# Kernel optimization log

Measured on AMD Instinct MI355X. Metric: run time of the kernel, lower is better.

The kernel has to match this reference:

```python
import jax, jax.numpy as jnp
import numpy as np

DIM = 144
HEADS = 6
HEAD_DIM = DIM // HEADS
SCALE = HEAD_DIM ** -0.5
WS = (2, 8, 8)  # (T, H, W); N = 2*8*8 = 128


def _rel_pos_index(ws):
    d, h, w = ws
    coords = np.stack(np.meshgrid(np.arange(d), np.arange(h), np.arange(w), indexing='ij'))
    cf = coords.reshape(3, -1)                      # (3, N)
    rc = (cf[:, :, None] - cf[:, None, :]).transpose(1, 2, 0)  # (N, N, 3)
    rc[..., 0] += d - 1
    rc[..., 1] += h - 1
    rc[..., 2] += w - 1
    rc[..., 0] *= (2 * h - 1) * (2 * w - 1)
    rc[..., 1] *= (2 * w - 1)
    return rc.sum(-1)                               # (N, N) int


def _sine_pos_encoding(hw, num_pos_feats, temperature=10000.0):
    # matches get_sine_position_encoding(..., normalize=True) -> (1, H*W, 2*num_pos_feats)
    H, W = hw
    scale = 2.0 * np.pi
    ones = np.ones((1, H, W), dtype=np.float64)
    y = np.cumsum(ones, 1)
    x = np.cumsum(ones, 2)
    eps = 1e-6
    y = y / (y[:, -1:, :] + eps) * scale
    x = x / (x[:, :, -1:] + eps) * scale
    dim_t = np.arange(num_pos_feats, dtype=np.float64)
    dim_t = temperature ** (2.0 * (dim_t // 2) / num_pos_feats)
    pos_x = x[..., None] / dim_t
    pos_y = y[..., None] / dim_t
    pos_x = np.stack((np.sin(pos_x[..., 0::2]), np.cos(pos_x[..., 1::2])), -1).reshape(1, H, W, -1)
    pos_y = np.stack((np.sin(pos_y[..., 0::2]), np.cos(pos_y[..., 1::2])), -1).reshape(1, H, W, -1)
    pos = np.concatenate((pos_y, pos_x), 3)         # (1, H, W, 2*npf)
    return pos.reshape(1, H * W, 2 * num_pos_feats).astype(np.float32)


RPI = _rel_pos_index(WS)                              # (128, 128) numpy int const
POS = _sine_pos_encoding(WS[1:], DIM // 2)            # (1, 64, 144) numpy const


def setup_inputs() -> dict:
    key = jax.random.key(0)
    ks = jax.random.split(key, 6)
    wB, N, C = 1024, 128, DIM
    return {
        'x': jax.random.normal(ks[0], (wB, N, C), jnp.float32),
        'rpb_table': 0.02 * jax.random.normal(ks[1], (675, HEADS), jnp.float32),
        'w_qkv_self': jax.random.normal(ks[2], (3 * C, C), jnp.float32) * (C ** -0.5),
        'w_qkv_mut': jax.random.normal(ks[3], (3 * C, C), jnp.float32) * (C ** -0.5),
        'w_proj': jax.random.normal(ks[4], (C, 2 * C), jnp.float32) * ((2 * C) ** -0.5),
        'b_proj': jax.random.normal(ks[5], (C,), jnp.float32) * 0.01,
    }


def _qkv(x, w):
    wB, N, C = x.shape
    qkv = (x @ w.T).reshape(wB, N, 3, HEADS, HEAD_DIM).transpose(2, 0, 3, 1, 4)
    return qkv[0], qkv[1], qkv[2]  # each (wB, heads, N, head_dim)


def _attention(q, k, v, rpb=None):
    # q,k,v: (wB, heads, n, head_dim)
    beta = jnp.einsum('bhnd,bhmd->bhnm', q * SCALE, k)
    if rpb is not None:
        beta = beta + rpb                             # (1, heads, n, n) broadcast
    alpha = jax.nn.softmax(beta, axis=-1)
    out = jnp.einsum('bhnm,bhmd->bhnd', alpha, v)
    wB, _, n, _ = q.shape
    return out.transpose(0, 2, 1, 3).reshape(wB, n, HEADS * HEAD_DIM)


def reference(x, rpb_table, w_qkv_self, w_qkv_mut, w_proj, b_proj):
    wB, N, C = x.shape
    # --- self attention with relative position bias ---
    q, k, v = _qkv(x, w_qkv_self)
    rpb = rpb_table[jnp.asarray(RPI.reshape(-1))].reshape(N, N, HEADS)
    rpb = rpb.transpose(2, 0, 1)[None]                # (1, heads, N, N)
    x_out = _attention(q, k, v, rpb)                  # (wB, N, C)
    # --- mutual attention between the two temporal halves ---
    pos = jnp.tile(jnp.asarray(POS, x.dtype), (1, 2, 1))  # (1, N, C)
    qm, km, vm = _qkv(x + pos, w_qkv_mut)
    half = N // 2
    q1, q2 = qm[:, :, :half], qm[:, :, half:]
    k1, k2 = km[:, :, :half], km[:, :, half:]
    v1, v2 = vm[:, :, :half], vm[:, :, half:]
    x1_aligned = _attention(q2, k1, v1)               # (wB, N/2, C)
    x2_aligned = _attention(q1, k2, v2)               # (wB, N/2, C)
    x_out = jnp.concatenate([jnp.concatenate([x1_aligned, x2_aligned], 1), x_out], 2)
    return x_out @ w_proj.T + b_proj                  # (wB, N, C)
```

## Files before the change

kernel.cpp:

```cpp
#include <hip/hip_runtime.h>

typedef float  f32x4 __attribute__((ext_vector_type(4)));
typedef short  s16x8 __attribute__((ext_vector_type(8)));
typedef short  s16x4 __attribute__((ext_vector_type(4)));

#define DEVI static __device__ __forceinline__

DEVI short f2b(float f) {
  unsigned u = __builtin_bit_cast(unsigned, f);
  unsigned r = (u + 0x7FFFu + ((u >> 16) & 1u)) >> 16;
  return (short)(unsigned short)r;
}
DEVI float b2f(short s) {
  unsigned u = ((unsigned)(unsigned short)s) << 16;
  return __builtin_bit_cast(float, u);
}
DEVI unsigned pk2(float lo, float hi) {
  unsigned a = __builtin_bit_cast(unsigned, lo) + 0x8000u;
  unsigned b = __builtin_bit_cast(unsigned, hi) + 0x8000u;
  return __builtin_amdgcn_perm(b, a, 0x07060302u);
}
DEVI s16x4 pack4(f32x4 v) {
  union { unsigned u[2]; s16x4 s; } t;
  t.u[0] = pk2(v[0], v[1]); t.u[1] = pk2(v[2], v[3]);
  return t.s;
}
DEVI s16x8 pack8(float4 a, float4 b) {
  union { unsigned u[4]; s16x8 s; } t;
  t.u[0] = pk2(a.x, a.y); t.u[1] = pk2(a.z, a.w);
  t.u[2] = pk2(b.x, b.y); t.u[3] = pk2(b.z, b.w);
  return t.s;
}

DEVI void stage16(const short* g, short* l) {
  __builtin_amdgcn_global_load_lds(
      (const __attribute__((address_space(1))) unsigned int*)g,
      (__attribute__((address_space(3))) unsigned int*)l, 16, 0, 0);
}

DEVI float pos_val(int n, int c) {
  int i = (n & 63) >> 3, j = n & 7;
  float base; int cc;
  if (c < 72) { base = (float)(i + 1); cc = c; }
  else        { base = (float)(j + 1); cc = c - 72; }
  int m = cc >> 1;
  const float SC  = (float)(6.283185307179586 / 8.000001);
  const float LNT = (float)(9.210340371976184 / 36.0);
  float arg = base * SC * __expf(-(float)m * LNT);
  return (cc & 1) ? cosf(arg) : sinf(arg);
}

__global__ void prep_kernel(const float* __restrict__ w_self,
                            const float* __restrict__ w_mut,
                            const float* __restrict__ w_proj,
                            const float* __restrict__ rpb_table,
                            short* WF, short* PF, float* RPF, short* POSB)
{
  const float SCALE = 0.20412414523193154f;
  const float LOG2E = 1.4426950408889634f;
  int b = blockIdx.x, l = threadIdx.x;
  if (b < 360) {
    int p = b / 180, r1 = b % 180, h = r1 / 30, r2 = r1 % 30, c = r2 / 5, ks = r2 % 5;
    const float* W = p ? w_mut : w_self;
    int strip = c >> 1, ct = c & 1;
    int d = ct * 16 + (l & 15);
    float sc = (strip == 0) ? SCALE * LOG2E : 1.0f;
    short* dst = WF + b * 512 + l * 8;
    #pragma unroll
    for (int j = 0; j < 8; ++j) {
      int k = ks * 32 + (l >> 4) * 8 + j;
      float v = (d < 24 && k < 144) ? W[(strip * 144 + h * 24 + d) * 144 + k] * sc : 0.f;
      dst[j] = f2b(v);
    }
  } else if (b < 468) {
    int b2 = b - 360, ct = b2 % 9, h = (b2 / 9) % 6, p = b2 / 54;
    int cf = ct * 16 + (l & 15);
    short* dst = PF + b2 * 512 + l * 8;
    #pragma unroll
    for (int j = 0; j < 8; ++j) {
      int d = (l >> 4) * 8 + j;
      float v = (d < 24) ? w_proj[cf * 288 + (p ? 0 : 144) + h * 24 + d] : 0.f;
      dst[j] = f2b(v);
    }
  } else if (b < 852) {
    int b3 = b - 468, mt = b3 % 8, w = (b3 / 8) % 8, h = b3 / 64;
    int n = w * 16 + (l & 15);
    int dn = n >> 6, hn = (n >> 3) & 7, wn = n & 7;
    f32x4 o;
    #pragma unroll
    for (int r = 0; r < 4; ++r) {
      int m = mt * 16 + ((l >> 4) << 2) + r;
      int dm = m >> 6, hm = (m >> 3) & 7, wm = m & 7;
      int idx = (dn - dm + 1) * 225 + (hn - hm + 7) * 15 + (wn - wm + 7);
      o[r] = rpb_table[idx * 6 + h] * LOG2E;
    }
    *reinterpret_cast<f32x4*>(RPF + b3 * 256 + l * 4) = o;
  } else {
    int e = (b - 852) * 64 + l;
    int n = e / 144, c = e - n * 144;
    POSB[e] = f2b(pos_val(n, c));
  }
}

template<int PATH>
DEVI void run_path(short* WB, short* PFB, short* QB, short* KB, short* VTb,
                   const short* WF, const short* PF, const float* RPF,
                   const s16x8 (&xf)[5], f32x4 (&oacc)[9],
                   int w, int lg, int ll, int l64)
{
  constexpr int NKS = PATH ? 2 : 4;
  const int mbase = PATH ? (w >> 2) * 64 : 0;
  const int qrow0 = (PATH ? (w ^ 4) : w) * 16;
  const f32x4 z4 = {0.f, 0.f, 0.f, 0.f};
  short* TP = QB + (w * 16) * 40;

  for (int h = 0; h < 6; ++h) {
    __syncthreads();
    #pragma unroll
    for (int c = 0; c < 6; ++c) {
      f32x4 acc = z4;
      #pragma unroll
      for (int ks = 0; ks < 5; ++ks) {
        s16x8 wa = *reinterpret_cast<const s16x8*>(&WB[(c * 5 + ks) * 512 + l64 * 8]);
        if (c < 4) acc = __builtin_amdgcn_mfma_f32_16x16x32_bf16(wa, xf[ks], acc, 0, 0, 0);
        else       acc = __builtin_amdgcn_mfma_f32_16x16x32_bf16(xf[ks], wa, acc, 0, 0, 0);
      }
      s16x4 o = pack4(acc);
      int ct = c & 1;
      if (c < 2)
        *reinterpret_cast<s16x4*>(&QB[(w * 16 + ll) * 40 + ct * 16 + lg * 4]) = o;
      else if (c < 4)
        *reinterpret_cast<s16x4*>(&KB[(w * 16 + ll) * 40 + ct * 16 + lg * 4]) = o;
      else
        *reinterpret_cast<s16x4*>(&VTb[(ct * 16 + ll) * 152 + w * 16 + lg * 4]) = o;
    }
    __syncthreads();
    s16x8 qf = *reinterpret_cast<const s16x8*>(&QB[(qrow0 + ll) * 40 + lg * 8]);
    if (PATH) __syncthreads();
    {
      const short* nwf = nullptr; const short* npf = nullptr;
      if (h < 5) {
        nwf = WF + (PATH * 6 + h + 1) * 30 * 512;
        npf = PF + (PATH * 6 + h + 1) * 9 * 512;
      } else if (PATH == 0) {
        nwf = WF + 6 * 30 * 512;
        npf = PF + 6 * 9 * 512;
      }
      if (nwf) {
        int nb = (h + 1) & 1;
        #pragma unroll
        for (int r = 0; r < 4; ++r) {
          int slot = r * 8 + w;
          if (slot < 30) stage16(nwf + slot * 512 + l64 * 8, WB + slot * 512);
        }
        #pragma unroll
        for (int r = 0; r < 2; ++r) {
          int slot = r * 8 + w;
          if (slot < 9) stage16(npf + slot * 512 + l64 * 8, PFB + nb * 4608 + slot * 512);
        }
      }
    }
    float vsum = 0.f;
    f32x4 pacc[2] = {z4, z4};
    #pragma unroll
    for (int ks = 0; ks < NKS; ++ks) {
      #pragma unroll
      for (int b2 = 0; b2 < 2; ++b2) {
        int mt = ks * 2 + b2;
        s16x8 kf = *reinterpret_cast<const s16x8*>(&KB[(mbase + mt * 16 + ll) * 40 + lg * 8]);
        f32x4 bb = __builtin_amdgcn_mfma_f32_16x16x32_bf16(kf, qf, z4, 0, 0, 0);
        f32x4 vv;
        if (PATH == 0) {
          f32x4 rp = *reinterpret_cast<const f32x4*>(RPF + (((h * 8 + w) * 8) + mt) * 256 + l64 * 4);
          #pragma unroll
          for (int r = 0; r < 4; ++r) vv[r] = __builtin_amdgcn_exp2f(bb[r] + rp[r]);
        } else {
          #pragma unroll
          for (int r = 0; r < 4; ++r) vv[r] = __builtin_amdgcn_exp2f(bb[r]);
        }
        vsum += (vv[0] + vv[1]) + (vv[2] + vv[3]);
        *reinterpret_cast<s16x4*>(&TP[ll * 40 + b2 * 16 + lg * 4]) = pack4(vv);
      }
      s16x8 af = *reinterpret_cast<const s16x8*>(&TP[ll * 40 + lg * 8]);
      #pragma unroll
      for (int dt = 0; dt < 2; ++dt) {
        s16x8 vf = *reinterpret_cast<const s16x8*>(&VTb[(dt * 16 + ll) * 152 + mbase + ks * 32 + lg * 8]);
        pacc[dt] = __builtin_amdgcn_mfma_f32_16x16x32_bf16(vf, af, pacc[dt], 0, 0, 0);
      }
    }
    vsum += __shfl_xor(vsum, 16, 64);
    vsum += __shfl_xor(vsum, 32, 64);
    float inv = 1.0f / vsum;
    #pragma unroll
    for (int dt = 0; dt < 2; ++dt) {
      f32x4 sc;
      #pragma unroll
      for (int r = 0; r < 4; ++r) sc[r] = pacc[dt][r] * inv;
      *reinterpret_cast<s16x4*>(&TP[ll * 40 + dt * 16 + lg * 4]) = pack4(sc);
    }
    {
      s16x8 of = *reinterpret_cast<const s16x8*>(&TP[ll * 40 + lg * 8]);
      const short* pfb = PFB + (h & 1) * 4608;
      #pragma unroll
      for (int ct = 0; ct < 9; ++ct) {
        s16x8 pf = *reinterpret_cast<const s16x8*>(&pfb[ct * 512 + l64 * 8]);
        oacc[ct] = __builtin_amdgcn_mfma_f32_16x16x32_bf16(of, pf, oacc[ct], 0, 0, 0);
      }
    }
  }
}

__global__ __launch_bounds__(512, 4)
void wmsa_kernel(const float* __restrict__ x,
                 const short* __restrict__ WF,
                 const short* __restrict__ PF,
                 const float* __restrict__ RPF,
                 const short* __restrict__ POSB,
                 const float* __restrict__ b_proj,
                 float* __restrict__ out)
{
  __shared__ short WB[30 * 512];
  __shared__ short PFB[2 * 9 * 512];
  __shared__ short QB[128 * 40];
  __shared__ short KB[128 * 40];
  __shared__ short VTb[32 * 152];

  const int tid = threadIdx.x;
  const int w   = tid >> 6;
  const int l64 = tid & 63;
  const int lg  = l64 >> 4;
  const int ll  = l64 & 15;
  const int blk = blockIdx.x;

  f32x4 oacc[9];
  const f32x4 z4 = {0.f, 0.f, 0.f, 0.f};
  #pragma unroll
  for (int i = 0; i < 9; ++i) oacc[i] = z4;

  #pragma unroll
  for (int r = 0; r < 4; ++r) {
    int slot = r * 8 + w;
    if (slot < 30) stage16(WF + slot * 512 + l64 * 8, WB + slot * 512);
  }
  #pragma unroll
  for (int r = 0; r < 2; ++r) {
    int slot = r * 8 + w;
    if (slot < 9) stage16(PF + slot * 512 + l64 * 8, PFB + slot * 512);
  }

  s16x8 xf[5];
  const float* xr = x + (size_t)blk * (128 * 144) + (w * 16 + ll) * 144 + lg * 8;
  #pragma unroll
  for (int ks = 0; ks < 5; ++ks) {
    s16x8 v = {0, 0, 0, 0, 0, 0, 0, 0};
    if (ks < 4 || lg < 2) {
      float4 a = *reinterpret_cast<const float4*>(xr + ks * 32);
      float4 b = *reinterpret_cast<const float4*>(xr + ks * 32 + 4);
      v = pack8(a, b);
    }
    xf[ks] = v;
  }

  run_path<0>(WB, PFB, QB, KB, VTb, WF, PF, RPF, xf, oacc, w, lg, ll, l64);

  {
    const short* pr = POSB + (w * 16 + ll) * 144 + lg * 8;
    #pragma unroll
    for (int ks = 0; ks < 5; ++ks) {
      if (ks < 4 || lg < 2) {
        s16x8 pv = *reinterpret_cast<const s16x8*>(pr + ks * 32);
        union { unsigned u[4]; s16x8 s; } t;
        #pragma unroll
        for (int j2 = 0; j2 < 4; ++j2) {
          float lo = b2f(xf[ks][2 * j2])     + b2f(pv[2 * j2]);
          float hi = b2f(xf[ks][2 * j2 + 1]) + b2f(pv[2 * j2 + 1]);
          t.u[j2] = pk2(lo, hi);
        }
        xf[ks] = t.s;
      }
    }
  }

  run_path<1>(WB, PFB, QB, KB, VTb, WF, PF, RPF, xf, oacc, w, lg, ll, l64);

  float* og = out + (size_t)blk * (128 * 144);
  #pragma unroll
  for (int ct = 0; ct < 9; ++ct) {
    int c = ct * 16 + ll;
    float bb = b_proj[c];
    #pragma unroll
    for (int r = 0; r < 4; ++r) {
      int n = w * 16 + lg * 4 + r;
      og[n * 144 + c] = oacc[ct][r] + bb;
    }
  }
}

extern "C" void kernel_launch(void* const* d_in, const int* in_sizes, int n_in,
                              void* d_out, int out_size, void* d_ws, size_t ws_size,
                              hipStream_t stream) {
  (void)in_sizes; (void)n_in; (void)out_size; (void)ws_size;
  const float* x   = (const float*)d_in[0];
  const float* rpb = (const float*)d_in[1];
  const float* wqs = (const float*)d_in[2];
  const float* wqm = (const float*)d_in[3];
  const float* wp  = (const float*)d_in[4];
  const float* bp  = (const float*)d_in[5];

  short* WF   = (short*)d_ws;
  short* PF   = WF + 360 * 512;
  float* RPF  = (float*)((char*)d_ws + 479232);
  short* POSB = (short*)((char*)d_ws + 872448);

  prep_kernel<<<dim3(1140), dim3(64), 0, stream>>>(wqs, wqm, wp, rpb, WF, PF, RPF, POSB);
  wmsa_kernel<<<dim3(1024), dim3(512), 0, stream>>>(x, WF, PF, RPF, POSB, bp, (float*)d_out);
}
```

Baseline: 131.9 us.

## Pack Q and K into shared 48-column tiles to cut padded QKV MFMAs

Q and K (24 columns each) were each padded to 32 columns, which took four 16-wide output tiles. They are now packed contiguously into 48 columns covered by three tiles, so QKV projection MFMAs per head drop from 30 to 25. Weight prep and staging shrink to 25 slots. Q/K now live in one 56-stride buffer with a zeroed pad region, and the attention probability scratch moves to a separate buffer. That removes the extra __syncthreads in the mutual path, at the cost of more LDS and a QK reduction over a packed fragment.

```diff
diff --git a/kernel.cpp b/kernel.cpp
--- a/kernel.cpp
+++ b/kernel.cpp
@@ -59,21 +59,28 @@
   const float SCALE = 0.20412414523193154f;
   const float LOG2E = 1.4426950408889634f;
   int b = blockIdx.x, l = threadIdx.x;
-  if (b < 360) {
-    int p = b / 180, r1 = b % 180, h = r1 / 30, r2 = r1 % 30, c = r2 / 5, ks = r2 % 5;
+  if (b < 300) {
+    int p = b / 150, r1 = b % 150, h = r1 / 25, r2 = r1 % 25, c = r2 / 5, ks = r2 % 5;
     const float* W = p ? w_mut : w_self;
-    int strip = c >> 1, ct = c & 1;
-    int d = ct * 16 + (l & 15);
-    float sc = (strip == 0) ? SCALE * LOG2E : 1.0f;
     short* dst = WF + b * 512 + l * 8;
     #pragma unroll
     for (int j = 0; j < 8; ++j) {
       int k = ks * 32 + (l >> 4) * 8 + j;
-      float v = (d < 24 && k < 144) ? W[(strip * 144 + h * 24 + d) * 144 + k] * sc : 0.f;
+      float v = 0.f;
+      if (k < 144) {
+        if (c < 3) {
+          int sc = c * 16 + (l & 15);
+          if (sc < 24) v = W[(h * 24 + sc) * 144 + k] * (SCALE * LOG2E);
+          else         v = W[(144 + h * 24 + (sc - 24)) * 144 + k];
+        } else {
+          int d = (c - 3) * 16 + (l & 15);
+          if (d < 24) v = W[(288 + h * 24 + d) * 144 + k];
+        }
+      }
       dst[j] = f2b(v);
     }
-  } else if (b < 468) {
-    int b2 = b - 360, ct = b2 % 9, h = (b2 / 9) % 6, p = b2 / 54;
+  } else if (b < 408) {
+    int b2 = b - 300, ct = b2 % 9, h = (b2 / 9) % 6, p = b2 / 54;
     int cf = ct * 16 + (l & 15);
     short* dst = PF + b2 * 512 + l * 8;
     #pragma unroll
@@ -82,8 +89,8 @@
       float v = (d < 24) ? w_proj[cf * 288 + (p ? 0 : 144) + h * 24 + d] : 0.f;
       dst[j] = f2b(v);
     }
-  } else if (b < 852) {
-    int b3 = b - 468, mt = b3 % 8, w = (b3 / 8) % 8, h = b3 / 64;
+  } else if (b < 792) {
+    int b3 = b - 408, mt = b3 % 8, w = (b3 / 8) % 8, h = b3 / 64;
     int n = w * 16 + (l & 15);
     int dn = n >> 6, hn = (n >> 3) & 7, wn = n & 7;
     f32x4 o;
@@ -96,14 +103,14 @@
     }
     *reinterpret_cast<f32x4*>(RPF + b3 * 256 + l * 4) = o;
   } else {
-    int e = (b - 852) * 64 + l;
+    int e = (b - 792) * 64 + l;
     int n = e / 144, c = e - n * 144;
     POSB[e] = f2b(pos_val(n, c));
   }
 }
 
 template<int PATH>
-DEVI void run_path(short* WB, short* PFB, short* QB, short* KB, short* VTb,
+DEVI void run_path(short* WB, short* PFB, short* QKB, short* VTb, short* AL,
                    const short* WF, const short* PF, const float* RPF,
                    const s16x8 (&xf)[5], f32x4 (&oacc)[9],
                    int w, int lg, int ll, int l64)
@@ -112,38 +119,35 @@
   const int mbase = PATH ? (w >> 2) * 64 : 0;
   const int qrow0 = (PATH ? (w ^ 4) : w) * 16;
   const f32x4 z4 = {0.f, 0.f, 0.f, 0.f};
-  short* TP = QB + (w * 16) * 40;
+  short* ALw = AL + (w * 16) * 40;
 
   for (int h = 0; h < 6; ++h) {
     __syncthreads();
     #pragma unroll
-    for (int c = 0; c < 6; ++c) {
+    for (int c = 0; c < 5; ++c) {
       f32x4 acc = z4;
       #pragma unroll
       for (int ks = 0; ks < 5; ++ks) {
         s16x8 wa = *reinterpret_cast<const s16x8*>(&WB[(c * 5 + ks) * 512 + l64 * 8]);
-        if (c < 4) acc = __builtin_amdgcn_mfma_f32_16x16x32_bf16(wa, xf[ks], acc, 0, 0, 0);
+        if (c < 3) acc = __builtin_amdgcn_mfma_f32_16x16x32_bf16(wa, xf[ks], acc, 0, 0, 0);
         else       acc = __builtin_amdgcn_mfma_f32_16x16x32_bf16(xf[ks], wa, acc, 0, 0, 0);
       }
       s16x4 o = pack4(acc);
-      int ct = c & 1;
-      if (c < 2)
-        *reinterpret_cast<s16x4*>(&QB[(w * 16 + ll) * 40 + ct * 16 + lg * 4]) = o;
-      else if (c < 4)
-        *reinterpret_cast<s16x4*>(&KB[(w * 16 + ll) * 40 + ct * 16 + lg * 4]) = o;
+      if (c < 3)
+        *reinterpret_cast<s16x4*>(&QKB[(w * 16 + ll) * 56 + c * 16 + lg * 4]) = o;
       else
-        *reinterpret_cast<s16x4*>(&VTb[(ct * 16 + ll) * 152 + w * 16 + lg * 4]) = o;
+        *reinterpret_cast<s16x4*>(&VTb[((c - 3) * 16 + ll) * 152 + w * 16 + lg * 4]) = o;
     }
     __syncthreads();
-    s16x8 qf = *reinterpret_cast<const s16x8*>(&QB[(qrow0 + ll) * 40 + lg * 8]);
-    if (PATH) __syncthreads();
+    s16x8 qf = {0, 0, 0, 0, 0, 0, 0, 0};
+    if (lg < 3) qf = *reinterpret_cast<const s16x8*>(&QKB[(qrow0 + ll) * 56 + lg * 8]);
     {
       const short* nwf = nullptr; const short* npf = nullptr;
       if (h < 5) {
-        nwf = WF + (PATH * 6 + h + 1) * 30 * 512;
+        nwf = WF + (PATH * 6 + h + 1) * 25 * 512;
         npf = PF + (PATH * 6 + h + 1) * 9 * 512;
       } else if (PATH == 0) {
-        nwf = WF + 6 * 30 * 512;
+        nwf = WF + 6 * 25 * 512;
         npf = PF + 6 * 9 * 512;
       }
       if (nwf) {
@@ -151,7 +155,7 @@
         #pragma unroll
         for (int r = 0; r < 4; ++r) {
           int slot = r * 8 + w;
-          if (slot < 30) stage16(nwf + slot * 512 + l64 * 8, WB + slot * 512);
+          if (slot < 25) stage16(nwf + slot * 512 + l64 * 8, WB + slot * 512);
         }
         #pragma unroll
         for (int r = 0; r < 2; ++r) {
@@ -167,7 +171,7 @@
       #pragma unroll
       for (int b2 = 0; b2 < 2; ++b2) {
         int mt = ks * 2 + b2;
-        s16x8 kf = *reinterpret_cast<const s16x8*>(&KB[(mbase + mt * 16 + ll) * 40 + lg * 8]);
+        s16x8 kf = *reinterpret_cast<const s16x8*>(&QKB[(mbase + mt * 16 + ll) * 56 + 24 + lg * 8]);
         f32x4 bb = __builtin_amdgcn_mfma_f32_16x16x32_bf16(kf, qf, z4, 0, 0, 0);
         f32x4 vv;
         if (PATH == 0) {
@@ -179,9 +183,9 @@
           for (int r = 0; r < 4; ++r) vv[r] = __builtin_amdgcn_exp2f(bb[r]);
         }
         vsum += (vv[0] + vv[1]) + (vv[2] + vv[3]);
-        *reinterpret_cast<s16x4*>(&TP[ll * 40 + b2 * 16 + lg * 4]) = pack4(vv);
-      }
-      s16x8 af = *reinterpret_cast<const s16x8*>(&TP[ll * 40 + lg * 8]);
+        *reinterpret_cast<s16x4*>(&ALw[ll * 40 + b2 * 16 + lg * 4]) = pack4(vv);
+      }
+      s16x8 af = *reinterpret_cast<const s16x8*>(&ALw[ll * 40 + lg * 8]);
       #pragma unroll
       for (int dt = 0; dt < 2; ++dt) {
         s16x8 vf = *reinterpret_cast<const s16x8*>(&VTb[(dt * 16 + ll) * 152 + mbase + ks * 32 + lg * 8]);
@@ -196,10 +200,10 @@
       f32x4 sc;
       #pragma unroll
       for (int r = 0; r < 4; ++r) sc[r] = pacc[dt][r] * inv;
-      *reinterpret_cast<s16x4*>(&TP[ll * 40 + dt * 16 + lg * 4]) = pack4(sc);
+      *reinterpret_cast<s16x4*>(&ALw[ll * 40 + dt * 16 + lg * 4]) = pack4(sc);
     }
     {
-      s16x8 of = *reinterpret_cast<const s16x8*>(&TP[ll * 40 + lg * 8]);
+      s16x8 of = *reinterpret_cast<const s16x8*>(&ALw[ll * 40 + lg * 8]);
       const short* pfb = PFB + (h & 1) * 4608;
       #pragma unroll
       for (int ct = 0; ct < 9; ++ct) {
@@ -219,11 +223,11 @@
                  const float* __restrict__ b_proj,
                  float* __restrict__ out)
 {
-  __shared__ short WB[30 * 512];
+  __shared__ short WB[25 * 512];
   __shared__ short PFB[2 * 9 * 512];
-  __shared__ short QB[128 * 40];
-  __shared__ short KB[128 * 40];
+  __shared__ short QKB[128 * 56];
   __shared__ short VTb[32 * 152];
+  __shared__ short AL[8 * 16 * 40];
 
   const int tid = threadIdx.x;
   const int w   = tid >> 6;
@@ -240,12 +244,16 @@
   #pragma unroll
   for (int r = 0; r < 4; ++r) {
     int slot = r * 8 + w;
-    if (slot < 30) stage16(WF + slot * 512 + l64 * 8, WB + slot * 512);
+    if (slot < 25) stage16(WF + slot * 512 + l64 * 8, WB + slot * 512);
   }
   #pragma unroll
   for (int r = 0; r < 2; ++r) {
     int slot = r * 8 + w;
     if (slot < 9) stage16(PF + slot * 512 + l64 * 8, PFB + slot * 512);
+  }
+  if (tid < 128) {
+    s16x8 zz = {0, 0, 0, 0, 0, 0, 0, 0};
+    *reinterpret_cast<s16x8*>(&QKB[tid * 56 + 48]) = zz;
   }
 
   s16x8 xf[5];
@@ -261,7 +269,7 @@
     xf[ks] = v;
   }
 
-  run_path<0>(WB, PFB, QB, KB, VTb, WF, PF, RPF, xf, oacc, w, lg, ll, l64);
+  run_path<0>(WB, PFB, QKB, VTb, AL, WF, PF, RPF, xf, oacc, w, lg, ll, l64);
 
   {
     const short* pr = POSB + (w * 16 + ll) * 144 + lg * 8;
@@ -281,7 +289,7 @@
     }
   }
 
-  run_path<1>(WB, PFB, QB, KB, VTb, WF, PF, RPF, xf, oacc, w, lg, ll, l64);
+  run_path<1>(WB, PFB, QKB, VTb, AL, WF, PF, RPF, xf, oacc, w, lg, ll, l64);
 
   float* og = out + (size_t)blk * (128 * 144);
   #pragma unroll
@@ -308,10 +316,10 @@
   const float* bp  = (const float*)d_in[5];
 
   short* WF   = (short*)d_ws;
-  short* PF   = WF + 360 * 512;
-  float* RPF  = (float*)((char*)d_ws + 479232);
-  short* POSB = (short*)((char*)d_ws + 872448);
-
-  prep_kernel<<<dim3(1140), dim3(64), 0, stream>>>(wqs, wqm, wp, rpb, WF, PF, RPF, POSB);
+  short* PF   = WF + 300 * 512;
+  float* RPF  = (float*)((char*)d_ws + 417792);
+  short* POSB = (short*)((char*)d_ws + 811008);
+
+  prep_kernel<<<dim3(1080), dim3(64), 0, stream>>>(wqs, wqm, wp, rpb, WF, PF, RPF, POSB);
   wmsa_kernel<<<dim3(1024), dim3(512), 0, stream>>>(x, WF, PF, RPF, POSB, bp, (float*)d_out);
 }
```

New measurement: 119.7 us. 9.2% less time.
